# Performance work log

Measured on AMD Instinct MI355X. Metric: run time of the kernel, lower is better.

## Reference

```python
import jax, jax.numpy as jnp
import numpy as np

N = 100000   # nodes
E = 1600000  # edges (avg degree 16)
F = 128      # input features
H = 64       # hidden_dim
C = 10       # num_classes
G = 128      # graphs in batch
EPS = 1e-5   # BatchNorm eps


def setup_inputs() -> dict:
    key = jax.random.key(0)
    ks = jax.random.split(key, 24)
    d = {}
    d['x'] = jax.random.normal(ks[0], (N, F), jnp.float32)
    d['edge_index'] = jax.random.randint(ks[1], (2, E), 0, N)
    d['batch'] = jnp.sort(jax.random.randint(ks[2], (N,), 0, G))
    # SAGEConv1: lin_l (aggregated, with bias) + lin_r (root, no bias)
    d['W1l'] = jax.random.normal(ks[3], (F, H), jnp.float32) * 0.05
    d['W1r'] = jax.random.normal(ks[4], (F, H), jnp.float32) * 0.05
    d['b1'] = jnp.zeros((H,), jnp.float32)
    # SAGEConv2
    d['W2l'] = jax.random.normal(ks[5], (H, H), jnp.float32) * 0.1
    d['W2r'] = jax.random.normal(ks[6], (H, H), jnp.float32) * 0.1
    d['b2'] = jnp.zeros((H,), jnp.float32)
    # BatchNorm (eval mode: running stats)
    for i, (kg, kb, km, kv) in enumerate([(7, 8, 9, 10), (11, 12, 13, 14), (15, 16, 17, 18)], 1):
        d[f'bn{i}_g'] = jax.random.uniform(ks[kg], (H,), jnp.float32, 0.5, 1.5)
        d[f'bn{i}_b'] = jax.random.normal(ks[kb], (H,), jnp.float32) * 0.1
        d[f'bn{i}_m'] = jax.random.normal(ks[km], (H,), jnp.float32) * 0.1
        d[f'bn{i}_v'] = jax.random.uniform(ks[kv], (H,), jnp.float32, 0.5, 1.5)
    # classifier head
    d['Wc1'] = jax.random.normal(ks[19], (H, H), jnp.float32) * 0.1
    d['bc1'] = jnp.zeros((H,), jnp.float32)
    d['Wc2'] = jax.random.normal(ks[20], (H, C), jnp.float32) * 0.1
    d['bc2'] = jnp.zeros((C,), jnp.float32)
    return d


def _bn(x, g, b, m, v):
    return (x - m) * jax.lax.rsqrt(v + EPS) * g + b


def _sage(x, src, dst, Wl, Wr, b):
    # mean aggregation of source-node features at destination nodes
    msum = jax.ops.segment_sum(x[src], dst, num_segments=N)          # [N, d]
    cnt = jax.ops.segment_sum(jnp.ones((E,), x.dtype), dst, num_segments=N)
    mean = msum / jnp.maximum(cnt, 1.0)[:, None]
    return mean @ Wl + b + x @ Wr


def reference(x, edge_index, batch,
              W1l, W1r, b1, W2l, W2r, b2,
              bn1_g, bn1_b, bn1_m, bn1_v,
              bn2_g, bn2_b, bn2_m, bn2_v,
              Wc1, bc1, bn3_g, bn3_b, bn3_m, bn3_v,
              Wc2, bc2):
    src, dst = edge_index[0], edge_index[1]
    h = _sage(x, src, dst, W1l, W1r, b1)
    h = jax.nn.relu(_bn(h, bn1_g, bn1_b, bn1_m, bn1_v))
    h = _sage(h, src, dst, W2l, W2r, b2)
    h = jax.nn.relu(_bn(h, bn2_g, bn2_b, bn2_m, bn2_v))
    # global mean pool over graphs
    gsum = jax.ops.segment_sum(h, batch, num_segments=G)             # [G, H]
    gcnt = jax.ops.segment_sum(jnp.ones((N,), h.dtype), batch, num_segments=G)
    g = gsum / jnp.maximum(gcnt, 1.0)[:, None]
    # classifier head (eval: dropout is identity)
    g = jax.nn.relu(_bn(g @ Wc1 + bc1, bn3_g, bn3_b, bn3_m, bn3_v))
    logits = g @ Wc2 + bc2
    return jax.nn.log_softmax(logits, axis=1)
```

## Files before the change

kernel.cpp:

```cpp
#include <hip/hip_runtime.h>
#include <hip/hip_bf16.h>
#include <math.h>

#define NN 100000
#define NE 1600000
#define FF 128
#define HH 64
#define CC 10
#define GG 128
#define BN_EPS 1e-5f

#define BNODES 64
#define NB 1563
#define PBLK 128
#define ECHUNK 12500
#define MHIST (NB * PBLK)
#define NSCAN 782
#define SCOL_CAP 2048

#define PNODES 16
#define POOL_BLOCKS 1563

typedef short v8bf __attribute__((ext_vector_type(8)));
typedef float v4f  __attribute__((ext_vector_type(4)));

__device__ inline ushort f2b(float x) {
    __hip_bfloat16 h = __float2bfloat16(x);
    return *reinterpret_cast<ushort*>(&h);
}
__device__ inline float b2f(ushort u) {
    return __uint_as_float(((unsigned)u) << 16);
}
__device__ inline float blo(unsigned u) { return __uint_as_float(u << 16); }
__device__ inline float bhi(unsigned u) { return __uint_as_float(u & 0xffff0000u); }

__device__ inline void sw_one(const float* __restrict__ W, ushort* __restrict__ o,
                              int t, int K) {
    const int lane = t & 63, nt = (t >> 6) & 3, ks = t >> 8;
    const int m = lane & 15, quad = lane >> 4;
#pragma unroll
    for (int j = 0; j < 8; ++j) {
        const int kk = ks * 32 + quad * 8 + j;
        const int cc = nt * 16 + m;
        o[t * 8 + j] = f2b(W[kk * 64 + cc]);
    }
}

__global__ __launch_bounds__(256) void prep_kernel(const float* __restrict__ W1l,
                                                   const float* __restrict__ W1r,
                                                   const float* __restrict__ W2l,
                                                   const float* __restrict__ W2r,
                                                   ushort* __restrict__ w1ls,
                                                   ushort* __restrict__ w1rs,
                                                   ushort* __restrict__ w2ls,
                                                   ushort* __restrict__ w2rs,
                                                   float* __restrict__ gz) {
    const int t = blockIdx.x * 256 + threadIdx.x;
    if (t < 1024) {
        sw_one(W1l, w1ls, t, FF);
        sw_one(W1r, w1rs, t, FF);
    } else if (t < 1536) {
        sw_one(W2l, w2ls, t - 1024, HH);
        sw_one(W2r, w2rs, t - 1024, HH);
    } else {
        for (int i = t - 1536; i < GG * 64 + GG; i += 512) gz[i] = 0.f;
    }
}

template<int K, int TPB, bool AF32>
__global__ __launch_bounds__(256) void gemm_mfma(const void* __restrict__ Xv,
                                                 const ushort* __restrict__ Bl,
                                                 const ushort* __restrict__ Br,
                                                 ushort* __restrict__ Yl,
                                                 ushort* __restrict__ Yr) {
    constexpr int KS = K / 32;
    const int lane  = threadIdx.x & 63;
    const int wave  = threadIdx.x >> 6;
    const int nhalf = wave & 1;
    const int rsub  = wave >> 1;
    const int m = lane & 15, quad = lane >> 4;

    v8bf bl[KS][2], br[KS][2];
#pragma unroll
    for (int ks = 0; ks < KS; ++ks)
#pragma unroll
        for (int nt = 0; nt < 2; ++nt) {
            const int nti = nhalf * 2 + nt;
            bl[ks][nt] = *(const v8bf*)(Bl + ((size_t)(ks * 4 + nti) * 64 + lane) * 8);
            br[ks][nt] = *(const v8bf*)(Br + ((size_t)(ks * 4 + nti) * 64 + lane) * 8);
        }

    for (int it = 0; it < TPB; ++it) {
        const int bt = blockIdx.x * TPB + it;
        const int row0 = bt * 32 + rsub * 16;
        if (row0 >= NN) return;
        const v4f z = {0.f, 0.f, 0.f, 0.f};
        v4f accl[2] = {z, z}, accr[2] = {z, z};
#pragma unroll
        for (int ks = 0; ks < KS; ++ks) {
            v8bf a;
            if (AF32) {
                const float* xrow = (const float*)Xv + (size_t)(row0 + m) * K + quad * 8 + ks * 32;
                const float4 a0 = *(const float4*)(xrow);
                const float4 a1 = *(const float4*)(xrow + 4);
                a[0] = (short)f2b(a0.x); a[1] = (short)f2b(a0.y);
                a[2] = (short)f2b(a0.z); a[3] = (short)f2b(a0.w);
                a[4] = (short)f2b(a1.x); a[5] = (short)f2b(a1.y);
                a[6] = (short)f2b(a1.z); a[7] = (short)f2b(a1.w);
            } else {
                const ushort* xrow = (const ushort*)Xv + (size_t)(row0 + m) * K + quad * 8 + ks * 32;
                a = *(const v8bf*)xrow;
            }
#pragma unroll
            for (int nt = 0; nt < 2; ++nt) {
                accl[nt] = __builtin_amdgcn_mfma_f32_16x16x32_bf16(a, bl[ks][nt], accl[nt], 0, 0, 0);
                accr[nt] = __builtin_amdgcn_mfma_f32_16x16x32_bf16(a, br[ks][nt], accr[nt], 0, 0, 0);
            }
        }
#pragma unroll
        for (int nt = 0; nt < 2; ++nt) {
            const int cc = nhalf * 32 + nt * 16 + m;
#pragma unroll
            for (int r = 0; r < 4; ++r) {
                const size_t off = (size_t)(row0 + quad * 4 + r) * 64 + cc;
                Yl[off] = f2b(accl[nt][r]);
                Yr[off] = f2b(accr[nt][r]);
            }
        }
    }
}

__global__ __launch_bounds__(1024) void edge_hist(const int* __restrict__ dst,
                                                  int* __restrict__ hist) {
    __shared__ int h[NB];
    for (int i = threadIdx.x; i < NB; i += 1024) h[i] = 0;
    __syncthreads();
    const int e0 = blockIdx.x * ECHUNK;
    for (int e = e0 + threadIdx.x; e < e0 + ECHUNK; e += 1024)
        atomicAdd(&h[dst[e] >> 6], 1);
    __syncthreads();
    for (int i = threadIdx.x; i < NB; i += 1024)
        hist[i * PBLK + blockIdx.x] = h[i];
}

__global__ __launch_bounds__(256) void scan_block(const int* __restrict__ cnt,
                                                  int* __restrict__ rp,
                                                  int* __restrict__ bsum) {
    __shared__ int s[256];
    const int tid = threadIdx.x;
    const int i = blockIdx.x * 256 + tid;
    const int v = (i < MHIST) ? cnt[i] : 0;
    s[tid] = v;
    __syncthreads();
    for (int off = 1; off < 256; off <<= 1) {
        int t = (tid >= off) ? s[tid - off] : 0;
        __syncthreads();
        s[tid] += t;
        __syncthreads();
    }
    if (i < MHIST) rp[i] = s[tid] - v;
    if (tid == 255) bsum[blockIdx.x] = s[255];
}

__global__ __launch_bounds__(256) void scan_bsums(const int* __restrict__ bsum,
                                                  int* __restrict__ boff) {
    __shared__ int s[256];
    const int tid = threadIdx.x;
    int v[4];
    int tot = 0;
#pragma unroll
    for (int j = 0; j < 4; ++j) {
        const int idx = tid * 4 + j;
        v[j] = (idx < NSCAN) ? bsum[idx] : 0;
        tot += v[j];
    }
    s[tid] = tot;
    __syncthreads();
    for (int off = 1; off < 256; off <<= 1) {
        int t = (tid >= off) ? s[tid - off] : 0;
        __syncthreads();
        s[tid] += t;
        __syncthreads();
    }
    int run = s[tid] - tot;
#pragma unroll
    for (int j = 0; j < 4; ++j) {
        const int idx = tid * 4 + j;
        if (idx < NSCAN) boff[idx] = run;
        run += v[j];
    }
}

__global__ __launch_bounds__(1024) void edge_scatter(const int* __restrict__ src,
                                                     const int* __restrict__ dst,
                                                     const int* __restrict__ goffs,
                                                     const int* __restrict__ boff,
                                                     int* __restrict__ pairs) {
    __shared__ int cur[NB];
    for (int i = threadIdx.x; i < NB; i += 1024) {
        const int idx = i * PBLK + blockIdx.x;
        cur[i] = goffs[idx] + boff[idx >> 8];
    }
    __syncthreads();
    const int e0 = blockIdx.x * ECHUNK;
    for (int e = e0 + threadIdx.x; e < e0 + ECHUNK; e += 1024) {
        const int s = src[e];
        const int d = dst[e];
        const int pos = atomicAdd(&cur[d >> 6], 1);
        pairs[pos] = (s << 6) | (d & (BNODES - 1));
    }
}

__global__ __launch_bounds__(256) void spmm_sorted(const int* __restrict__ goffs,
                                                   const int* __restrict__ boff,
                                                   const int* __restrict__ pairs,
                                                   const ushort* __restrict__ Yl,
                                                   const ushort* __restrict__ Yr,
                                                   const float* __restrict__ bias,
                                                   const float* __restrict__ bng,
                                                   const float* __restrict__ bnb,
                                                   const float* __restrict__ bnm,
                                                   const float* __restrict__ bnv,
                                                   ushort* __restrict__ outp) {
    __shared__ int scol[SCOL_CAP];
    __shared__ int deg[BNODES];
    __shared__ int loffs[BNODES];
    __shared__ int fill[BNODES];
    const int tid = threadIdx.x;
    const int b = blockIdx.x;

    if (tid < BNODES) { deg[tid] = 0; fill[tid] = 0; }
    __syncthreads();

    const int beg = goffs[b * PBLK] + boff[b >> 1];
    int end = (b == NB - 1) ? NE : goffs[(b + 1) * PBLK] + boff[(b + 1) >> 1];
    if (end - beg > SCOL_CAP) end = beg + SCOL_CAP;

    int pv[8];
    int npv = 0;
    for (int i = beg + tid; i < end; i += 256) {
        const int v = pairs[i];
        pv[npv++] = v;
        atomicAdd(&deg[v & (BNODES - 1)], 1);
    }
    __syncthreads();

    if (tid < BNODES) loffs[tid] = deg[tid];
    __syncthreads();
    for (int s = 1; s < BNODES; s <<= 1) {
        int v = 0;
        if (tid < BNODES && tid >= s) v = loffs[tid - s];
        __syncthreads();
        if (tid < BNODES) loffs[tid] += v;
        __syncthreads();
    }

    for (int j = 0; j < npv; ++j) {
        const int v = pv[j];
        const int dl = v & (BNODES - 1);
        const int pos = (loffs[dl] - deg[dl]) + atomicAdd(&fill[dl], 1);
        scol[pos] = v >> 6;
    }
    __syncthreads();

    const int wv = tid >> 6, lane = tid & 63;
    const int grp = lane >> 3, subl = lane & 7;

    float biasj[8], scj[8], mj[8], bbj[8];
#pragma unroll
    for (int j = 0; j < 8; ++j) {
        const int ch = subl * 8 + j;
        biasj[j] = bias[ch];
        scj[j] = bng[ch] * rsqrtf(bnv[ch] + BN_EPS);
        mj[j] = bnm[ch];
        bbj[j] = bnb[ch];
    }

    for (int i = 0; i < 2; ++i) {
        const int nl = wv * 16 + i * 8 + grp;
        const int node = b * BNODES + nl;
        if (node >= NN) continue;
        const int dg = deg[nl];
        const int nbeg = loffs[nl] - dg;
        const int nend = nbeg + dg;
        float a[8] = {0.f, 0.f, 0.f, 0.f, 0.f, 0.f, 0.f, 0.f};
        float c[8] = {0.f, 0.f, 0.f, 0.f, 0.f, 0.f, 0.f, 0.f};
        int e = nbeg;
        for (; e + 1 < nend; e += 2) {
            const int s0 = scol[e];
            const int s1 = scol[e + 1];
            const uint4 r0 = *(const uint4*)(Yl + (size_t)s0 * 64 + subl * 8);
            const uint4 r1 = *(const uint4*)(Yl + (size_t)s1 * 64 + subl * 8);
            a[0] += blo(r0.x); a[1] += bhi(r0.x); a[2] += blo(r0.y); a[3] += bhi(r0.y);
            a[4] += blo(r0.z); a[5] += bhi(r0.z); a[6] += blo(r0.w); a[7] += bhi(r0.w);
            c[0] += blo(r1.x); c[1] += bhi(r1.x); c[2] += blo(r1.y); c[3] += bhi(r1.y);
            c[4] += blo(r1.z); c[5] += bhi(r1.z); c[6] += blo(r1.w); c[7] += bhi(r1.w);
        }
        if (e < nend) {
            const int s0 = scol[e];
            const uint4 r0 = *(const uint4*)(Yl + (size_t)s0 * 64 + subl * 8);
            a[0] += blo(r0.x); a[1] += bhi(r0.x); a[2] += blo(r0.y); a[3] += bhi(r0.y);
            a[4] += blo(r0.z); a[5] += bhi(r0.z); a[6] += blo(r0.w); a[7] += bhi(r0.w);
        }
        const float inv = 1.0f / fmaxf((float)dg, 1.0f);
        const uint4 yr = *(const uint4*)(Yr + (size_t)node * 64 + subl * 8);
        float hj[8];
        hj[0] = (a[0] + c[0]) * inv + biasj[0] + blo(yr.x);
        hj[1] = (a[1] + c[1]) * inv + biasj[1] + bhi(yr.x);
        hj[2] = (a[2] + c[2]) * inv + biasj[2] + blo(yr.y);
        hj[3] = (a[3] + c[3]) * inv + biasj[3] + bhi(yr.y);
        hj[4] = (a[4] + c[4]) * inv + biasj[4] + blo(yr.z);
        hj[5] = (a[5] + c[5]) * inv + biasj[5] + bhi(yr.z);
        hj[6] = (a[6] + c[6]) * inv + biasj[6] + blo(yr.w);
        hj[7] = (a[7] + c[7]) * inv + biasj[7] + bhi(yr.w);
        unsigned ow[4];
#pragma unroll
        for (int j = 0; j < 4; ++j) {
            const float o0 = fmaxf((hj[2 * j] - mj[2 * j]) * scj[2 * j] + bbj[2 * j], 0.0f);
            const float o1 = fmaxf((hj[2 * j + 1] - mj[2 * j + 1]) * scj[2 * j + 1] + bbj[2 * j + 1], 0.0f);
            ow[j] = (unsigned)f2b(o0) | ((unsigned)f2b(o1) << 16);
        }
        uint4 o;
        o.x = ow[0]; o.y = ow[1]; o.z = ow[2]; o.w = ow[3];
        *(uint4*)(outp + (size_t)node * 64 + subl * 8) = o;
    }
}

__global__ __launch_bounds__(256) void pool_seg(const ushort* __restrict__ h,
                                                const int* __restrict__ batch,
                                                float* __restrict__ gsum,
                                                float* __restrict__ gcnt) {
    const int wave = blockIdx.x * 4 + (threadIdx.x >> 6);
    const int lane = threadIdx.x & 63;
    const int n0 = wave * PNODES;
    if (n0 >= NN) return;
    const int n1 = (n0 + PNODES < NN) ? n0 + PNODES : NN;
    int g = batch[n0];
    float acc = 0.f, c = 0.f;
#pragma unroll 4
    for (int n = n0; n < n1; ++n) {
        const int b = batch[n];
        if (b != g) {
            atomicAdd(&gsum[g * 64 + lane], acc);
            if (lane == 0) atomicAdd(&gcnt[g], c);
            acc = 0.f; c = 0.f; g = b;
        }
        acc += b2f(h[(size_t)n * 64 + lane]);
        c += 1.0f;
    }
    atomicAdd(&gsum[g * 64 + lane], acc);
    if (lane == 0) atomicAdd(&gcnt[g], c);
}

__global__ __launch_bounds__(64) void head_kernel(const float* __restrict__ gsum,
                                                  const float* __restrict__ gcnt,
                                                  const float* __restrict__ Wc1,
                                                  const float* __restrict__ bc1,
                                                  const float* __restrict__ g3,
                                                  const float* __restrict__ b3,
                                                  const float* __restrict__ m3,
                                                  const float* __restrict__ v3,
                                                  const float* __restrict__ Wc2,
                                                  const float* __restrict__ bc2,
                                                  float* __restrict__ out) {
    __shared__ float sg[64];
    __shared__ float st[64];
    __shared__ float sl[10];
    __shared__ float sls;
    const int b = blockIdx.x;
    const int c = threadIdx.x;
    sg[c] = gsum[b * 64 + c] / fmaxf(gcnt[b], 1.0f);
    __syncthreads();
    float acc = bc1[c];
#pragma unroll
    for (int k = 0; k < 64; ++k) acc += sg[k] * Wc1[k * 64 + c];
    const float sc = g3[c] * rsqrtf(v3[c] + BN_EPS);
    st[c] = fmaxf((acc - m3[c]) * sc + b3[c], 0.0f);
    __syncthreads();
    if (c < CC) {
        float lg = bc2[c];
#pragma unroll
        for (int k = 0; k < 64; ++k) lg += st[k] * Wc2[k * CC + c];
        sl[c] = lg;
    }
    __syncthreads();
    if (c == 0) {
        float mx = sl[0];
        for (int i = 1; i < CC; ++i) mx = fmaxf(mx, sl[i]);
        float s = 0.f;
        for (int i = 0; i < CC; ++i) s += expf(sl[i] - mx);
        sls = mx + logf(s);
    }
    __syncthreads();
    if (c < CC) out[b * CC + c] = sl[c] - sls;
}

extern "C" void kernel_launch(void* const* d_in, const int* in_sizes, int n_in,
                              void* d_out, int out_size, void* d_ws, size_t ws_size,
                              hipStream_t stream) {
    const float* x    = (const float*)d_in[0];
    const int*   ei   = (const int*)d_in[1];
    const int*   batch= (const int*)d_in[2];
    const float* W1l  = (const float*)d_in[3];
    const float* W1r  = (const float*)d_in[4];
    const float* b1   = (const float*)d_in[5];
    const float* W2l  = (const float*)d_in[6];
    const float* W2r  = (const float*)d_in[7];
    const float* b2   = (const float*)d_in[8];
    const float* bn1g = (const float*)d_in[9];
    const float* bn1b = (const float*)d_in[10];
    const float* bn1m = (const float*)d_in[11];
    const float* bn1v = (const float*)d_in[12];
    const float* bn2g = (const float*)d_in[13];
    const float* bn2b = (const float*)d_in[14];
    const float* bn2m = (const float*)d_in[15];
    const float* bn2v = (const float*)d_in[16];
    const float* bn3g = (const float*)d_in[17];
    const float* bn3b = (const float*)d_in[18];
    const float* bn3m = (const float*)d_in[19];
    const float* bn3v = (const float*)d_in[20];
    const float* Wc1  = (const float*)d_in[21];
    const float* bc1  = (const float*)d_in[22];
    const float* Wc2  = (const float*)d_in[23];
    const float* bc2  = (const float*)d_in[24];
    float* out = (float*)d_out;

    const int* src = ei;
    const int* dst = ei + NE;

    char* p = (char*)d_ws;
    ushort* yl   = (ushort*)p;                 p += (size_t)NN * 64 * 2;
    ushort* yr   = (ushort*)p;                 p += (size_t)NN * 64 * 2;
    ushort* hbuf = (ushort*)p;                 p += (size_t)NN * 64 * 2;
    int*    pairs= (int*)p;                    p += (size_t)NE * 4;
    int*    hist = (int*)p;                    p += (size_t)MHIST * 4;
    int*    goffs= (int*)p;                    p += (size_t)MHIST * 4;
    int*    bsum = (int*)p;                    p += 1024 * 4;
    int*    boff = (int*)p;                    p += 1024 * 4;
    ushort* w1ls = (ushort*)p;                 p += (size_t)FF * 64 * 2;
    ushort* w1rs = (ushort*)p;                 p += (size_t)FF * 64 * 2;
    ushort* w2ls = (ushort*)p;                 p += (size_t)HH * 64 * 2;
    ushort* w2rs = (ushort*)p;                 p += (size_t)HH * 64 * 2;
    float* gsum  = (float*)p;                  p += (size_t)GG * 64 * 4;
    float* gcnt  = gsum + GG * 64;             p += (size_t)GG * 4;

    edge_hist<<<PBLK, 1024, 0, stream>>>(dst, hist);
    scan_block<<<NSCAN, 256, 0, stream>>>(hist, goffs, bsum);
    scan_bsums<<<1, 256, 0, stream>>>(bsum, boff);
    edge_scatter<<<PBLK, 1024, 0, stream>>>(src, dst, goffs, boff, pairs);

    prep_kernel<<<8, 256, 0, stream>>>(W1l, W1r, W2l, W2r, w1ls, w1rs, w2ls, w2rs, gsum);

    gemm_mfma<FF, 2, true><<<1563, 256, 0, stream>>>((const void*)x, w1ls, w1rs, yl, yr);
    spmm_sorted<<<NB, 256, 0, stream>>>(goffs, boff, pairs, yl, yr, b1,
                                        bn1g, bn1b, bn1m, bn1v, hbuf);

    gemm_mfma<HH, 2, false><<<1563, 256, 0, stream>>>((const void*)hbuf, w2ls, w2rs, yl, yr);
    spmm_sorted<<<NB, 256, 0, stream>>>(goffs, boff, pairs, yl, yr, b2,
                                        bn2g, bn2b, bn2m, bn2v, hbuf);

    pool_seg<<<POOL_BLOCKS, 256, 0, stream>>>(hbuf, batch, gsum, gcnt);
    head_kernel<<<GG, 64, 0, stream>>>(gsum, gcnt, Wc1, bc1,
                                       bn3g, bn3b, bn3m, bn3v, Wc2, bc2, out);
}
```

Measured before the change: 290.3 us.

## Stage edge scatter through LDS for coalesced writes; use wave-shuffle scans

The edge scatter now performs a local counting sort of each block's edge chunk in shared memory, then writes pairs to their global positions in a contiguous sweep. This is meant to replace the scattered 4-byte global stores, which hit random bucket positions, with writes that mostly land in runs per bucket. The two scan kernels swap their log-step shared-memory scans with barriers for wavefront shuffle-up scans plus a small cross-wave combine, which cuts barrier count. The new scatter uses about 112KB of LDS per block, which limits occupancy to one block per CU, and adds extra hist reads.

```diff
diff --git a/kernel.cpp b/kernel.cpp
--- a/kernel.cpp
+++ b/kernel.cpp
@@ -146,26 +146,31 @@
 __global__ __launch_bounds__(256) void scan_block(const int* __restrict__ cnt,
                                                   int* __restrict__ rp,
                                                   int* __restrict__ bsum) {
-    __shared__ int s[256];
+    __shared__ int ws[4];
     const int tid = threadIdx.x;
+    const int lane = tid & 63, wv = tid >> 6;
     const int i = blockIdx.x * 256 + tid;
     const int v = (i < MHIST) ? cnt[i] : 0;
-    s[tid] = v;
-    __syncthreads();
-    for (int off = 1; off < 256; off <<= 1) {
-        int t = (tid >= off) ? s[tid - off] : 0;
-        __syncthreads();
-        s[tid] += t;
-        __syncthreads();
-    }
-    if (i < MHIST) rp[i] = s[tid] - v;
-    if (tid == 255) bsum[blockIdx.x] = s[255];
+    int inc = v;
+#pragma unroll
+    for (int off = 1; off < 64; off <<= 1) {
+        int t = __shfl_up(inc, off, 64);
+        if (lane >= off) inc += t;
+    }
+    if (lane == 63) ws[wv] = inc;
+    __syncthreads();
+    int wbase = 0;
+#pragma unroll
+    for (int w = 0; w < 4; ++w) wbase += (w < wv) ? ws[w] : 0;
+    if (i < MHIST) rp[i] = wbase + inc - v;
+    if (tid == 255) bsum[blockIdx.x] = wbase + inc;
 }
 
 __global__ __launch_bounds__(256) void scan_bsums(const int* __restrict__ bsum,
                                                   int* __restrict__ boff) {
-    __shared__ int s[256];
+    __shared__ int ws[4];
     const int tid = threadIdx.x;
+    const int lane = tid & 63, wv = tid >> 6;
     int v[4];
     int tot = 0;
 #pragma unroll
@@ -174,15 +179,18 @@
         v[j] = (idx < NSCAN) ? bsum[idx] : 0;
         tot += v[j];
     }
-    s[tid] = tot;
-    __syncthreads();
-    for (int off = 1; off < 256; off <<= 1) {
-        int t = (tid >= off) ? s[tid - off] : 0;
-        __syncthreads();
-        s[tid] += t;
-        __syncthreads();
-    }
-    int run = s[tid] - tot;
+    int inc = tot;
+#pragma unroll
+    for (int off = 1; off < 64; off <<= 1) {
+        int t = __shfl_up(inc, off, 64);
+        if (lane >= off) inc += t;
+    }
+    if (lane == 63) ws[wv] = inc;
+    __syncthreads();
+    int wbase = 0;
+#pragma unroll
+    for (int w = 0; w < 4; ++w) wbase += (w < wv) ? ws[w] : 0;
+    int run = wbase + inc - tot;
 #pragma unroll
     for (int j = 0; j < 4; ++j) {
         const int idx = tid * 4 + j;
@@ -193,21 +201,61 @@
 
 __global__ __launch_bounds__(1024) void edge_scatter(const int* __restrict__ src,
                                                      const int* __restrict__ dst,
+                                                     const int* __restrict__ hist,
                                                      const int* __restrict__ goffs,
                                                      const int* __restrict__ boff,
                                                      int* __restrict__ pairs) {
-    __shared__ int cur[NB];
-    for (int i = threadIdx.x; i < NB; i += 1024) {
-        const int idx = i * PBLK + blockIdx.x;
-        cur[i] = goffs[idx] + boff[idx >> 8];
-    }
-    __syncthreads();
-    const int e0 = blockIdx.x * ECHUNK;
-    for (int e = e0 + threadIdx.x; e < e0 + ECHUNK; e += 1024) {
+    __shared__ int sv[ECHUNK];
+    __shared__ int sd[ECHUNK];
+    __shared__ int sfill[NB];
+    __shared__ int sdelta[NB];
+    __shared__ int wsum[16];
+    const int tid = threadIdx.x;
+    const int lane = tid & 63, wv = tid >> 6;
+    const int p = blockIdx.x;
+
+    int c0 = 0, c1 = 0, g0 = 0, g1 = 0;
+    const int i0 = 2 * tid, i1 = 2 * tid + 1;
+    if (i0 < NB) {
+        const int idx = i0 * PBLK + p;
+        c0 = hist[idx];
+        g0 = goffs[idx] + boff[idx >> 8];
+    }
+    if (i1 < NB) {
+        const int idx = i1 * PBLK + p;
+        c1 = hist[idx];
+        g1 = goffs[idx] + boff[idx >> 8];
+    }
+    const int tv = c0 + c1;
+    int inc = tv;
+#pragma unroll
+    for (int off = 1; off < 64; off <<= 1) {
+        int t = __shfl_up(inc, off, 64);
+        if (lane >= off) inc += t;
+    }
+    if (lane == 63) wsum[wv] = inc;
+    __syncthreads();
+    int wbase = 0;
+#pragma unroll
+    for (int w = 0; w < 16; ++w) wbase += (w < wv) ? wsum[w] : 0;
+    const int excl = wbase + inc - tv;
+    if (i0 < NB) { sfill[i0] = excl;      sdelta[i0] = g0 - excl; }
+    if (i1 < NB) { sfill[i1] = excl + c0; sdelta[i1] = g1 - (excl + c0); }
+    __syncthreads();
+
+    const int e0 = p * ECHUNK;
+    for (int e = e0 + tid; e < e0 + ECHUNK; e += 1024) {
         const int s = src[e];
         const int d = dst[e];
-        const int pos = atomicAdd(&cur[d >> 6], 1);
-        pairs[pos] = (s << 6) | (d & (BNODES - 1));
+        const int b = d >> 6;
+        const int local = atomicAdd(&sfill[b], 1);
+        sv[local] = (s << 6) | (d & (BNODES - 1));
+        sd[local] = local + sdelta[b];
+    }
+    __syncthreads();
+
+    for (int j = tid; j < ECHUNK; j += 1024) {
+        pairs[sd[j]] = sv[j];
     }
 }
 
@@ -447,7 +495,7 @@
     edge_hist<<<PBLK, 1024, 0, stream>>>(dst, hist);
     scan_block<<<NSCAN, 256, 0, stream>>>(hist, goffs, bsum);
     scan_bsums<<<1, 256, 0, stream>>>(bsum, boff);
-    edge_scatter<<<PBLK, 1024, 0, stream>>>(src, dst, goffs, boff, pairs);
+    edge_scatter<<<PBLK, 1024, 0, stream>>>(src, dst, hist, goffs, boff, pairs);
 
     prep_kernel<<<8, 256, 0, stream>>>(W1l, W1r, W2l, W2r, w1ls, w1rs, w2ls, w2rs, gsum);
 
```

New measurement: 286.0 us. About the same (-1.5%).
